# Kernel tuning notes

Measured on AMD Instinct MI355X. Metric: run time of the kernel, lower is better.

Reference implementation:

```python
import jax, jax.numpy as jnp
import numpy as np

B, S, D, H = 2, 2048, 768, 12
DH = D // H  # head dim = 64


def setup_inputs() -> dict:
    key = jax.random.key(0)
    ks = jax.random.split(key, 4)
    query = jax.random.normal(ks[0], (B, S, D), dtype=jnp.float32)
    # right-padding: positions >= length are padded (True = masked)
    lengths = jax.random.randint(ks[1], (B,), S // 2, S + 1)
    padding_mask = jnp.arange(S)[None, :] >= lengths[:, None]
    w_qkv = jax.random.normal(ks[2], (3 * D, D), dtype=jnp.float32) * 0.02
    b_qkv = jnp.zeros((3 * D,), dtype=jnp.float32)
    w_out = jax.random.normal(ks[3], (D, D), dtype=jnp.float32) * 0.02
    b_out = jnp.zeros((D,), dtype=jnp.float32)
    return {"query": query, "padding_mask": padding_mask, "w_qkv": w_qkv,
            "b_qkv": b_qkv, "w_out": w_out, "b_out": b_out}


def reference(query, padding_mask, w_qkv, b_qkv, w_out, b_out):
    # qkv_same self-attention path, future_mask=True, dropout in eval mode.
    qkv = query @ w_qkv.T + b_qkv                       # [B,S,3D]
    q, k, v = jnp.split(qkv, 3, axis=-1)
    split = lambda x: x.reshape(B, S, H, DH).transpose(0, 2, 1, 3)  # [B,H,S,dh]
    q, k, v = split(q), split(k), split(v)
    scale = jnp.float32(1.0 / np.sqrt(DH))
    w = jnp.einsum('bhqd,bhkd->bhqk', q, k) * scale     # [B,H,S,S]
    neg_inf = jnp.float32(-jnp.inf)
    causal = jnp.triu(jnp.ones((S, S), dtype=bool), 1)  # strict upper = future
    w = jnp.where(causal[None, None], neg_inf, w)
    w = jnp.where(padding_mask[:, None, None, :], neg_inf, w)
    # rows where every key is masked -> output zeros (matches torch cleanup)
    all_masked = jnp.all(jnp.isneginf(w), axis=-1)      # [B,H,S]
    w = jnp.where(all_masked[..., None], 0.0, w)        # avoid NaN in softmax
    p = jax.nn.softmax(w, axis=-1)
    p = jnp.where(all_masked[..., None], 0.0, p)
    out = jnp.einsum('bhqk,bhkd->bhqd', p, v)           # [B,H,S,dh]
    out = out.transpose(0, 2, 1, 3).reshape(B, S, D)
    return out @ w_out.T + b_out
```

## Files before the change

kernel.cpp:

```cpp
#include <hip/hip_runtime.h>

#define BATCH 2
#define SEQ 2048
#define DMODEL 768
#define NH 12
#define DHEAD 64
#define D3 (3 * DMODEL)

typedef float f32x4 __attribute__((ext_vector_type(4)));
typedef __bf16 bf16x8 __attribute__((ext_vector_type(8)));
typedef __bf16 bf16x4 __attribute__((ext_vector_type(4)));

#define NEG_INF (-__builtin_inff())
#define SCL 0.18033688011112042f

__device__ __forceinline__ void g2l16(const void* g, void* l) {
    __builtin_amdgcn_global_load_lds(
        (const __attribute__((address_space(1))) void*)g,
        (__attribute__((address_space(3))) void*)l,
        16, 0, 0);
}

__device__ __forceinline__ unsigned pack_bf16(float lo, float hi) {
    unsigned a = __builtin_bit_cast(unsigned short, (__bf16)lo);
    unsigned b = __builtin_bit_cast(unsigned short, (__bf16)hi);
    return a | (b << 16);
}

#define XQ 786432
#define WQQ 442368
#define WOQ 147456
#define WQROWS 147456
__global__ __launch_bounds__(256) void cvt3_kernel(const float* __restrict__ X,
                                                   const float* __restrict__ Wq,
                                                   const float* __restrict__ Wo,
                                                   __bf16* __restrict__ Xb,
                                                   __bf16* __restrict__ Wqb,
                                                   __bf16* __restrict__ Wob) {
    int i = blockIdx.x * 256 + threadIdx.x;
    const float* s; __bf16* d; int k;
    float scl = 1.0f;
    if (i < XQ)            { s = X;  d = Xb;  k = i; }
    else if (i < XQ + WQQ) { s = Wq; d = Wqb; k = i - XQ; if (k < WQROWS) scl = SCL; }
    else                   { s = Wo; d = Wob; k = i - XQ - WQQ; }
    float4 v = ((const float4*)s)[k];
    bf16x4 o;
    o[0] = (__bf16)(v.x * scl); o[1] = (__bf16)(v.y * scl);
    o[2] = (__bf16)(v.z * scl); o[3] = (__bf16)(v.w * scl);
    ((bf16x4*)d)[k] = o;
}

__global__ __launch_bounds__(256) void lens_kernel(const unsigned char* __restrict__ mask,
                                                   const float* __restrict__ bq,
                                                   float* __restrict__ bqs,
                                                   int* __restrict__ lens) {
    __shared__ int nz_s;
    __shared__ int cnt[2];
    if (threadIdx.x == 0) { nz_s = 0; cnt[0] = 0; cnt[1] = 0; }
    __syncthreads();
    for (int i = threadIdx.x; i < D3; i += 256)
        bqs[i] = bq[i] * (i < DMODEL ? SCL : 1.0f);
    uint4 mv = ((const uint4*)mask)[threadIdx.x];
    if (mv.x | mv.y | mv.z | mv.w) nz_s = 1;
    __syncthreads();
    int c0 = 0, c1 = 0;
    if (nz_s) {
        for (int s = threadIdx.x; s < SEQ; s += 256) {
            c0 += (mask[s] != 0);
            c1 += (mask[SEQ + s] != 0);
        }
    } else {
        const int* mi = (const int*)mask;
        for (int s = threadIdx.x; s < SEQ; s += 256) {
            c0 += (mi[s] != 0);
            c1 += (mi[SEQ + s] != 0);
        }
    }
    atomicAdd(&cnt[0], c0);
    atomicAdd(&cnt[1], c1);
    __syncthreads();
    if (threadIdx.x == 0) {
        lens[0] = SEQ - cnt[0];
        lens[1] = SEQ - cnt[1];
    }
}

__global__ __launch_bounds__(256) void gemm_qkv(const __bf16* __restrict__ A,
                                                const __bf16* __restrict__ Bw,
                                                const float* __restrict__ bias,
                                                __bf16* __restrict__ Qd,
                                                __bf16* __restrict__ Kd,
                                                __bf16* __restrict__ Vp) {
    const int K = 768;
    __shared__ __align__(16) __bf16 As[128][64];
    __shared__ __align__(16) __bf16 Bs[128][64];
    const int tid = threadIdx.x;
    const int wave = tid >> 6, lane = tid & 63;
    const int bm = blockIdx.x * 128, bn = blockIdx.y * 128;
    const int wr = (wave >> 1) * 64, wc = (wave & 1) * 64;
    const int l15 = lane & 15, lg = lane >> 4;
    const int rsub = lane >> 3;
    const int csub = (((lane & 7) ^ rsub) * 8);
    const int rswz = (l15 & 7) * 8;

    f32x4 acc[4][4] = {};

    for (int kt = 0; kt < K; kt += 64) {
#pragma unroll
        for (int it = 0; it < 4; ++it) {
            int c = it * 4 + wave;
            int row = c * 8 + rsub;
            g2l16(A + (size_t)(bm + row) * K + kt + csub, &As[0][0] + c * 512);
            g2l16(Bw + (size_t)(bn + row) * K + kt + csub, &Bs[0][0] + c * 512);
        }
        __syncthreads();
#pragma unroll
        for (int kk = 0; kk < 2; ++kk) {
            bf16x8 af[4], bfr[4];
            const int col = (kk * 32 + lg * 8) ^ rswz;
#pragma unroll
            for (int m = 0; m < 4; ++m)
                af[m] = *(const bf16x8*)(&As[0][0] + (wr + m * 16 + l15) * 64 + col);
#pragma unroll
            for (int n = 0; n < 4; ++n)
                bfr[n] = *(const bf16x8*)(&Bs[0][0] + (wc + n * 16 + l15) * 64 + col);
#pragma unroll
            for (int m = 0; m < 4; ++m)
#pragma unroll
                for (int n = 0; n < 4; ++n)
                    acc[m][n] = __builtin_amdgcn_mfma_f32_16x16x32_bf16(af[m], bfr[n], acc[m][n], 0, 0, 0);
        }
        __syncthreads();
    }

#pragma unroll
    for (int n = 0; n < 4; ++n) {
        int col = bn + wc + n * 16 + l15;
        float bv = bias[col];
#pragma unroll
        for (int m = 0; m < 4; ++m) {
#pragma unroll
            for (int j = 0; j < 4; ++j) {
                int row = bm + wr + m * 16 + lg * 4 + j;
                __bf16 v = (__bf16)(acc[m][n][j] + bv);
                if (bn < 768) {
                    Qd[(size_t)row * 768 + col] = v;
                } else if (bn < 1536) {
                    int kc = col - 768;
                    int hh = kc >> 6, dh = kc & 63;
                    int bb = row >> 11, key = row & 2047;
                    Kd[(size_t)(bb * NH + hh) * 131072 + key * 64 + dh] = v;
                } else {
                    int vc = col - 1536;
                    int hh = vc >> 6, dh = vc & 63;
                    int bb = row >> 11, key = row & 2047;
                    Vp[(size_t)(bb * NH + hh) * 131072 + (key >> 6) * 4096 + dh * 64 + (key & 63)] = v;
                }
            }
        }
    }
}

__global__ __launch_bounds__(256) void gemm_out(const __bf16* __restrict__ A,
                                                const __bf16* __restrict__ Bw,
                                                const float* __restrict__ bias,
                                                float* __restrict__ Cout,
                                                int M, int N, int K) {
    __shared__ __align__(16) __bf16 As[128][64];
    __shared__ __align__(16) __bf16 Bs[128][64];
    const int tid = threadIdx.x;
    const int wave = tid >> 6, lane = tid & 63;
    const int bm = blockIdx.x * 128, bn = blockIdx.y * 128;
    const int wr = (wave >> 1) * 64, wc = (wave & 1) * 64;
    const int l15 = lane & 15, lg = lane >> 4;
    const int rsub = lane >> 3;
    const int csub = (((lane & 7) ^ rsub) * 8);
    const int rswz = (l15 & 7) * 8;

    f32x4 acc[4][4] = {};

    for (int kt = 0; kt < K; kt += 64) {
#pragma unroll
        for (int it = 0; it < 4; ++it) {
            int c = it * 4 + wave;
            int row = c * 8 + rsub;
            g2l16(A + (size_t)(bm + row) * K + kt + csub, &As[0][0] + c * 512);
            g2l16(Bw + (size_t)(bn + row) * K + kt + csub, &Bs[0][0] + c * 512);
        }
        __syncthreads();
#pragma unroll
        for (int kk = 0; kk < 2; ++kk) {
            bf16x8 af[4], bfr[4];
            const int col = (kk * 32 + lg * 8) ^ rswz;
#pragma unroll
            for (int m = 0; m < 4; ++m)
                af[m] = *(const bf16x8*)(&As[0][0] + (wr + m * 16 + l15) * 64 + col);
#pragma unroll
            for (int n = 0; n < 4; ++n)
                bfr[n] = *(const bf16x8*)(&Bs[0][0] + (wc + n * 16 + l15) * 64 + col);
#pragma unroll
            for (int m = 0; m < 4; ++m)
#pragma unroll
                for (int n = 0; n < 4; ++n)
                    acc[m][n] = __builtin_amdgcn_mfma_f32_16x16x32_bf16(af[m], bfr[n], acc[m][n], 0, 0, 0);
        }
        __syncthreads();
    }

#pragma unroll
    for (int n = 0; n < 4; ++n) {
        int col = bn + wc + n * 16 + l15;
        float bv = bias[col];
#pragma unroll
        for (int m = 0; m < 4; ++m) {
#pragma unroll
            for (int j = 0; j < 4; ++j) {
                int row = bm + wr + m * 16 + lg * 4 + j;
                Cout[(size_t)row * N + col] = acc[m][n][j] + bv;
            }
        }
    }
}

__global__ __launch_bounds__(128) void attn_kernel(const __bf16* __restrict__ Qd,
                                                   const __bf16* __restrict__ Kd,
                                                   const int* __restrict__ lens,
                                                   const __bf16* __restrict__ Vp,
                                                   __bf16* __restrict__ Out) {
    const int lane = threadIdx.x & 63, wave = threadIdx.x >> 6;
    const int l15 = lane & 15, lg = lane >> 4;
    const int blk = blockIdx.x;
    const int xcd = blk & 7, idx = blk >> 3;
    const int hl = idx % 3, pd2 = idx / 3;
    const int p = 63 - (pd2 * 2 + wave);
    const int bh = xcd * 3 + hl;
    const int b = bh / NH, h = bh % NH;
    const int len = lens[b];
    const int q0 = p * 32;

    const int prow = ((l15 >> 2) << 3) + (l15 & 3);
    const __bf16* kbase = Kd + (size_t)bh * 131072 + prow * 64 + lg * 8;
    const __bf16* vbase = Vp + (size_t)bh * 131072 + l15 * 64 + lg * 8;

    bf16x8 qf[2][2];
    int qcap[2];
#pragma unroll
    for (int m = 0; m < 2; ++m) {
        const __bf16* qp_ = Qd + (size_t)(b * SEQ + q0 + m * 16 + l15) * DMODEL + h * DHEAD + lg * 8;
        qf[m][0] = *(const bf16x8*)qp_;
        qf[m][1] = *(const bf16x8*)(qp_ + 32);
        int myq = q0 + m * 16 + l15;
        qcap[m] = (len - 1 < myq) ? (len - 1) : myq;
    }

    int kmax = q0 + 32;
    if (len < kmax) kmax = len;
    const int nt = (kmax + 63) >> 6;

    f32x4 accO[2][4] = {};
    float l_part[2] = {0.f, 0.f};

    bf16x8 kA[2][4], kB[2][4];
    f32x4 scA[2][4], scB[2][4];

    auto kload = [&](bf16x8(&kf)[2][4], int kt) {
        const int k0 = kt * 64;
#pragma unroll
        for (int n = 0; n < 4; ++n) {
            const int roff = (k0 + ((n >> 1) << 5) + ((n & 1) << 2)) * 64;
#pragma unroll
            for (int kkd = 0; kkd < 2; ++kkd)
                kf[kkd][n] = *(const bf16x8*)(kbase + roff + kkd * 32);
        }
    };

    auto qk = [&](f32x4(&sc)[2][4], bf16x8(&kf)[2][4]) {
        __builtin_amdgcn_s_setprio(1);
#pragma unroll
        for (int m = 0; m < 2; ++m)
#pragma unroll
            for (int n = 0; n < 4; ++n) {
                sc[m][n] = __builtin_amdgcn_mfma_f32_16x16x32_bf16(kf[0][n], qf[m][0],
                                                                   f32x4{0.f, 0.f, 0.f, 0.f}, 0, 0, 0);
                sc[m][n] = __builtin_amdgcn_mfma_f32_16x16x32_bf16(kf[1][n], qf[m][1], sc[m][n], 0, 0, 0);
            }
        __builtin_amdgcn_s_setprio(0);
    };

    auto step = [&](f32x4(&sc)[2][4], int kt) {
        const int k0 = kt * 64;
        const __bf16* vt = vbase + kt * 4096;
        bf16x8 vf[2][4];
#pragma unroll
        for (int kk = 0; kk < 2; ++kk)
#pragma unroll
            for (int n = 0; n < 4; ++n)
                vf[kk][n] = *(const bf16x8*)(vt + n * 1024 + kk * 32);

        bf16x8 pa[2][2];
#pragma unroll
        for (int m = 0; m < 2; ++m) {
            const bool full = (k0 + 63 <= q0 + m * 16) && (k0 + 63 < len);
            float psum = 0.f;
            unsigned pk[4][2];
#pragma unroll
            for (int n = 0; n < 4; ++n) {
                const int keyb = k0 + ((n >> 1) << 5) + lg * 8 + ((n & 1) << 2);
                float pv[4];
#pragma unroll
                for (int j = 0; j < 4; ++j) {
                    float e = exp2f(sc[m][n][j]);
                    if (!full) e = (keyb + j <= qcap[m]) ? e : 0.f;
                    pv[j] = e;
                }
                psum += (pv[0] + pv[1]) + (pv[2] + pv[3]);
                pk[n][0] = pack_bf16(pv[0], pv[1]);
                pk[n][1] = pack_bf16(pv[2], pv[3]);
            }
            l_part[m] += psum;

            uint4 u0 = {pk[0][0], pk[0][1], pk[1][0], pk[1][1]};
            uint4 u1 = {pk[2][0], pk[2][1], pk[3][0], pk[3][1]};
            pa[m][0] = __builtin_bit_cast(bf16x8, u0);
            pa[m][1] = __builtin_bit_cast(bf16x8, u1);
        }

        __builtin_amdgcn_s_setprio(1);
#pragma unroll
        for (int m = 0; m < 2; ++m)
#pragma unroll
            for (int kk = 0; kk < 2; ++kk)
#pragma unroll
                for (int n = 0; n < 4; ++n)
                    accO[m][n] = __builtin_amdgcn_mfma_f32_16x16x32_bf16(pa[m][kk], vf[kk][n], accO[m][n], 0, 0, 0);
        __builtin_amdgcn_s_setprio(0);
    };

    kload(kA, 0);
    qk(scA, kA);
    if (nt > 1) kload(kB, 1);

    int t = 0;
    for (;;) {
        {
            const bool hasN = (t + 1 < nt);
            if (hasN) qk(scB, kB);
            if (t + 2 < nt) kload(kA, t + 2);
            step(scA, t);
            ++t;
            if (!hasN) break;
        }
        {
            const bool hasN = (t + 1 < nt);
            if (hasN) qk(scA, kA);
            if (t + 2 < nt) kload(kB, t + 2);
            step(scB, t);
            ++t;
            if (!hasN) break;
        }
    }

#pragma unroll
    for (int m = 0; m < 2; ++m) {
        float lp = l_part[m];
        lp += __shfl_xor(lp, 16);
        lp += __shfl_xor(lp, 32);
        float inv = 1.0f / lp;
        float inv_j[4];
#pragma unroll
        for (int j = 0; j < 4; ++j) inv_j[j] = __shfl(inv, lg * 4 + j);
#pragma unroll
        for (int n = 0; n < 4; ++n)
#pragma unroll
            for (int j = 0; j < 4; ++j) {
                int q = q0 + m * 16 + lg * 4 + j;
                Out[(size_t)(b * SEQ + q) * DMODEL + h * DHEAD + n * 16 + l15] =
                    (__bf16)(accO[m][n][j] * inv_j[j]);
            }
    }
}

extern "C" void kernel_launch(void* const* d_in, const int* in_sizes, int n_in,
                              void* d_out, int out_size, void* d_ws, size_t ws_size,
                              hipStream_t stream) {
    const float* query = (const float*)d_in[0];
    const unsigned char* mask = (const unsigned char*)d_in[1];
    const float* w_qkv = (const float*)d_in[2];
    const float* b_qkv = (const float*)d_in[3];
    const float* w_out = (const float*)d_in[4];
    const float* b_out = (const float*)d_in[5];
    float* out = (float*)d_out;

    if (ws_size < 36200448ull) return;
    char* p = (char*)d_ws;
    int* lens = (int*)p;        p += 256;
    float* bqs = (float*)p;     p += 2304 * 4 + 256;
    __bf16* Xb = (__bf16*)p;    p += (size_t)4096 * 768 * 2;
    __bf16* Wqb = (__bf16*)p;   p += (size_t)2304 * 768 * 2;
    __bf16* Wob = (__bf16*)p;   p += (size_t)768 * 768 * 2;
    __bf16* Qd = (__bf16*)p;    p += (size_t)4096 * 768 * 2;
    __bf16* Kd = (__bf16*)p;    p += (size_t)4096 * 768 * 2;
    __bf16* Vp = (__bf16*)p;    p += (size_t)4096 * 768 * 2;
    __bf16* AOb = (__bf16*)p;   p += (size_t)4096 * 768 * 2;

    lens_kernel<<<1, 256, 0, stream>>>(mask, b_qkv, bqs, lens);
    cvt3_kernel<<<(XQ + WQQ + WOQ) / 256, 256, 0, stream>>>(query, w_qkv, w_out, Xb, Wqb, Wob);

    gemm_qkv<<<dim3(32, 18), 256, 0, stream>>>(Xb, Wqb, bqs, Qd, Kd, Vp);
    attn_kernel<<<768, 128, 0, stream>>>(Qd, Kd, lens, Vp, AOb);
    gemm_out<<<dim3(32, 6), 256, 0, stream>>>(AOb, Wob, b_out, out, 4096, 768, 768);
}
```

Baseline: 135.0 us.

## Share K/V tiles across four waves via swizzled LDS double buffering

The attention kernel now runs 4 waves per block covering 128 query rows. K and V tiles are staged once per block into XOR-swizzled shared memory with async global-to-LDS loads and double buffering, instead of each wave loading its own fragments straight from global memory into registers. This cuts redundant global and L2 traffic and overlaps loads with compute. In exchange it adds block-wide barriers every tile, and causal imbalance means early waves sit idle while later waves finish their extra tiles.

```diff
diff --git a/kernel.cpp b/kernel.cpp
--- a/kernel.cpp
+++ b/kernel.cpp
@@ -222,25 +222,30 @@
     }
 }
 
-__global__ __launch_bounds__(128) void attn_kernel(const __bf16* __restrict__ Qd,
+__global__ __launch_bounds__(256) void attn_kernel(const __bf16* __restrict__ Qd,
                                                    const __bf16* __restrict__ Kd,
                                                    const int* __restrict__ lens,
                                                    const __bf16* __restrict__ Vp,
                                                    __bf16* __restrict__ Out) {
+    __shared__ __align__(16) __bf16 KT[2][4096];
+    __shared__ __align__(16) __bf16 VT[2][4096];
+
     const int lane = threadIdx.x & 63, wave = threadIdx.x >> 6;
     const int l15 = lane & 15, lg = lane >> 4;
     const int blk = blockIdx.x;
     const int xcd = blk & 7, idx = blk >> 3;
-    const int hl = idx % 3, pd2 = idx / 3;
-    const int p = 63 - (pd2 * 2 + wave);
+    const int hl = idx % 3, qbd = idx / 3;
+    const int qb = 15 - qbd;
     const int bh = xcd * 3 + hl;
     const int b = bh / NH, h = bh % NH;
     const int len = lens[b];
-    const int q0 = p * 32;
-
-    const int prow = ((l15 >> 2) << 3) + (l15 & 3);
-    const __bf16* kbase = Kd + (size_t)bh * 131072 + prow * 64 + lg * 8;
-    const __bf16* vbase = Vp + (size_t)bh * 131072 + l15 * 64 + lg * 8;
+    const int q0b = qb * 128;
+    const int q0 = q0b + wave * 32;
+
+    const __bf16* Ktile0 = Kd + (size_t)bh * 131072;
+    const __bf16* Vtile0 = Vp + (size_t)bh * 131072;
+
+    const int lr = lane >> 3, lc = lane & 7;
 
     bf16x8 qf[2][2];
     int qcap[2];
@@ -253,28 +258,56 @@
         qcap[m] = (len - 1 < myq) ? (len - 1) : myq;
     }
 
-    int kmax = q0 + 32;
+    int kmax = q0b + 128;
     if (len < kmax) kmax = len;
     const int nt = (kmax + 63) >> 6;
+    int mymax = q0 + 32;
+    if (len < mymax) mymax = len;
+    const int mynt = (mymax + 63) >> 6;
+
+    const int prow = ((l15 >> 2) << 3) + (l15 & 3);
+    int koff[2][4], voff[2][4];
+#pragma unroll
+    for (int n = 0; n < 4; ++n) {
+        int tr = ((n >> 1) << 5) + ((n & 1) << 2) + prow;
+        int sw = ((tr ^ (tr >> 3)) & 7) << 4;
+#pragma unroll
+        for (int kk = 0; kk < 2; ++kk)
+            koff[kk][n] = tr * 128 + ((kk * 64 + lg * 16) ^ sw);
+        int tv = n * 16 + l15;
+        int sv = ((tv ^ (tv >> 3)) & 7) << 4;
+#pragma unroll
+        for (int kk = 0; kk < 2; ++kk)
+            voff[kk][n] = tv * 128 + ((kk * 64 + lg * 16) ^ sv);
+    }
 
     f32x4 accO[2][4] = {};
     float l_part[2] = {0.f, 0.f};
 
-    bf16x8 kA[2][4], kB[2][4];
-    f32x4 scA[2][4], scB[2][4];
-
-    auto kload = [&](bf16x8(&kf)[2][4], int kt) {
-        const int k0 = kt * 64;
-#pragma unroll
-        for (int n = 0; n < 4; ++n) {
-            const int roff = (k0 + ((n >> 1) << 5) + ((n & 1) << 2)) * 64;
-#pragma unroll
-            for (int kkd = 0; kkd < 2; ++kkd)
-                kf[kkd][n] = *(const bf16x8*)(kbase + roff + kkd * 32);
+    auto stage = [&](int buf, int t) {
+#pragma unroll
+        for (int i = 0; i < 2; ++i) {
+            int c = wave * 2 + i;
+            int r = c * 8 + lr;
+            int srcoff = r * 64 + 8 * (lc ^ ((lr ^ c) & 7));
+            g2l16(Ktile0 + t * 4096 + srcoff, &KT[buf][0] + c * 512);
+            g2l16(Vtile0 + t * 4096 + srcoff, &VT[buf][0] + c * 512);
         }
     };
 
-    auto qk = [&](f32x4(&sc)[2][4], bf16x8(&kf)[2][4]) {
+    auto compute = [&](int buf, int t) {
+        const int k0 = t * 64;
+        const char* kb = (const char*)&KT[buf][0];
+        const char* vb = (const char*)&VT[buf][0];
+
+        bf16x8 kf[2][4];
+#pragma unroll
+        for (int kk = 0; kk < 2; ++kk)
+#pragma unroll
+            for (int n = 0; n < 4; ++n)
+                kf[kk][n] = *(const bf16x8*)(kb + koff[kk][n]);
+
+        f32x4 sc[2][4];
         __builtin_amdgcn_s_setprio(1);
 #pragma unroll
         for (int m = 0; m < 2; ++m)
@@ -285,17 +318,13 @@
                 sc[m][n] = __builtin_amdgcn_mfma_f32_16x16x32_bf16(kf[1][n], qf[m][1], sc[m][n], 0, 0, 0);
             }
         __builtin_amdgcn_s_setprio(0);
-    };
-
-    auto step = [&](f32x4(&sc)[2][4], int kt) {
-        const int k0 = kt * 64;
-        const __bf16* vt = vbase + kt * 4096;
+
         bf16x8 vf[2][4];
 #pragma unroll
         for (int kk = 0; kk < 2; ++kk)
 #pragma unroll
             for (int n = 0; n < 4; ++n)
-                vf[kk][n] = *(const bf16x8*)(vt + n * 1024 + kk * 32);
+                vf[kk][n] = *(const bf16x8*)(vb + voff[kk][n]);
 
         bf16x8 pa[2][2];
 #pragma unroll
@@ -336,28 +365,13 @@
         __builtin_amdgcn_s_setprio(0);
     };
 
-    kload(kA, 0);
-    qk(scA, kA);
-    if (nt > 1) kload(kB, 1);
-
-    int t = 0;
-    for (;;) {
-        {
-            const bool hasN = (t + 1 < nt);
-            if (hasN) qk(scB, kB);
-            if (t + 2 < nt) kload(kA, t + 2);
-            step(scA, t);
-            ++t;
-            if (!hasN) break;
-        }
-        {
-            const bool hasN = (t + 1 < nt);
-            if (hasN) qk(scA, kA);
-            if (t + 2 < nt) kload(kB, t + 2);
-            step(scB, t);
-            ++t;
-            if (!hasN) break;
-        }
+    stage(0, 0);
+    __syncthreads();
+    for (int t = 0; t < nt; ++t) {
+        const int cur = t & 1;
+        if (t + 1 < nt) stage(cur ^ 1, t + 1);
+        if (t < mynt) compute(cur, t);
+        __syncthreads();
     }
 
 #pragma unroll
@@ -407,6 +421,6 @@
     cvt3_kernel<<<(XQ + WQQ + WOQ) / 256, 256, 0, stream>>>(query, w_qkv, w_out, Xb, Wqb, Wob);
 
     gemm_qkv<<<dim3(32, 18), 256, 0, stream>>>(Xb, Wqb, bqs, Qd, Kd, Vp);
-    attn_kernel<<<768, 128, 0, stream>>>(Qd, Kd, lens, Vp, AOb);
+    attn_kernel<<<384, 256, 0, stream>>>(Qd, Kd, lens, Vp, AOb);
     gemm_out<<<dim3(32, 6), 256, 0, stream>>>(AOb, Wob, b_out, out, 4096, 768, 768);
 }
```

Result: slower. 144.4 us (+7.0%).
